# Optimization experiments

Measured on AMD Instinct MI355X. Metric: run time of the kernel, lower is better.

The kernel has to match this reference:

```python
import jax, jax.numpy as jnp
import numpy as np

# output_shape = (batch, channels, ny, nx)
B, C, NY, NX = 16, 64, 400, 400
NV_PER_BATCH = 12000  # non-empty pillars per frame (typical PointPillars)


def setup_inputs() -> dict:
    rng = np.random.default_rng(0)
    # unique pillar cells per batch -> deterministic scatter (matches torch last-write)
    cells = np.stack([rng.choice(NY * NX, NV_PER_BATCH, replace=False) for _ in range(B)])  # (B, NV)
    b_col = np.repeat(np.arange(B), NV_PER_BATCH)
    y = (cells // NX).reshape(-1)
    x = (cells % NX).reshape(-1)
    z = np.zeros_like(x)
    batched_indices = jnp.asarray(np.stack([b_col, z, y, x], axis=1), dtype=jnp.int32)  # (N, 4)
    voxel_features = jax.random.normal(jax.random.key(0), (B * NV_PER_BATCH, C), dtype=jnp.float32)
    return {"voxel_features": voxel_features, "batched_indices": batched_indices}


def reference(voxel_features, batched_indices):
    # fused global flat index: (batch, y, x) -> b*ny*nx + y*nx + x
    b = batched_indices[:, 0].astype(jnp.int32)
    y = batched_indices[:, 2].astype(jnp.int32)
    x = batched_indices[:, 3].astype(jnp.int32)
    flat = b * (NY * NX) + y * NX + x  # (N,)
    canvas = jnp.zeros((B * NY * NX, voxel_features.shape[1]), dtype=voxel_features.dtype)
    canvas = canvas.at[flat].set(voxel_features, unique_indices=True)
    # (B*NY*NX, C) -> (B, C, NY, NX)
    return canvas.reshape(B, NY, NX, -1).transpose(0, 3, 1, 2)
```

## Files before the change

kernel.cpp:

```cpp
#include <hip/hip_runtime.h>


constexpr int BATCH = 16;
constexpr int CH    = 64;
constexpr int NYD   = 400;
constexpr int NXD   = 400;
constexpr int NYNX  = NYD * NXD;
constexpr int SLABS = 8;
constexpr int CPS   = CH / SLABS;
constexpr int TILE  = 2048;

typedef float f4 __attribute__((ext_vector_type(4)));

__global__ void scatter_map_kernel(const int4* __restrict__ idx,
                                   unsigned short* __restrict__ map, int n, int nv) {
    int i = blockIdx.x * blockDim.x + threadIdx.x;
    if (i < n) {
        int4 v = idx[i];
        map[v.x * NYNX + v.z * NXD + v.w] = (unsigned short)(i - v.x * nv);
    }
}

__global__ __launch_bounds__(256)
void gather_kernel(const float* __restrict__ feat,
                   const unsigned short* __restrict__ map,
                   float* __restrict__ out, int nv) {
    const int b    = blockIdx.y;
    const int c0   = blockIdx.z * CPS;
    const int base = blockIdx.x * TILE + threadIdx.x * 4;

    const unsigned short* mapb  = map + (size_t)b * NYNX;
    const float*          featb = feat + ((size_t)b * nv) * CH + c0;
    float*                outb  = out + ((size_t)b * CH + c0) * NYNX;
    const f4 z4 = {0.f, 0.f, 0.f, 0.f};

    bool gv[2];
    unsigned short js[2][4];
    f4 f[2][4][2];
    #pragma unroll
    for (int g = 0; g < 2; ++g) {
        const int yx = base + g * 1024;
        gv[g] = (yx < NYNX);
        ushort4 m = gv[g] ? *reinterpret_cast<const ushort4*>(mapb + yx)
                          : make_ushort4(0xFFFFu, 0xFFFFu, 0xFFFFu, 0xFFFFu);
        js[g][0] = m.x; js[g][1] = m.y; js[g][2] = m.z; js[g][3] = m.w;
        #pragma unroll
        for (int cc = 0; cc < 4; ++cc) {
            if (js[g][cc] != 0xFFFFu) {
                const f4* src = reinterpret_cast<const f4*>(featb + (size_t)js[g][cc] * CH);
                f[g][cc][0] = src[0];
                f[g][cc][1] = src[1];
            } else {
                f[g][cc][0] = z4;
                f[g][cc][1] = z4;
            }
        }
    }

    #pragma unroll
    for (int g = 0; g < 2; ++g) {
        if (!gv[g]) continue;
        const int yx = base + g * 1024;
        #pragma unroll
        for (int k = 0; k < 2; ++k) {
            f4 r0 = {f[g][0][k].x, f[g][1][k].x, f[g][2][k].x, f[g][3][k].x};
            f4 r1 = {f[g][0][k].y, f[g][1][k].y, f[g][2][k].y, f[g][3][k].y};
            f4 r2 = {f[g][0][k].z, f[g][1][k].z, f[g][2][k].z, f[g][3][k].z};
            f4 r3 = {f[g][0][k].w, f[g][1][k].w, f[g][2][k].w, f[g][3][k].w};
            __builtin_nontemporal_store(r0, reinterpret_cast<f4*>(outb + (size_t)(4 * k + 0) * NYNX + yx));
            __builtin_nontemporal_store(r1, reinterpret_cast<f4*>(outb + (size_t)(4 * k + 1) * NYNX + yx));
            __builtin_nontemporal_store(r2, reinterpret_cast<f4*>(outb + (size_t)(4 * k + 2) * NYNX + yx));
            __builtin_nontemporal_store(r3, reinterpret_cast<f4*>(outb + (size_t)(4 * k + 3) * NYNX + yx));
        }
    }
}

__global__ void zero_kernel(float4* __restrict__ out, int n4) {
    int i = blockIdx.x * blockDim.x + threadIdx.x;
    if (i < n4) out[i] = make_float4(0.f, 0.f, 0.f, 0.f);
}

__global__ void direct_scatter_kernel(const float* __restrict__ feat,
                                      const int4* __restrict__ idx,
                                      float* __restrict__ out, int n) {
    int i = blockIdx.x * (blockDim.x / CH) + threadIdx.x / CH;
    int c = threadIdx.x % CH;
    if (i < n) {
        int4 v = idx[i];
        out[(size_t)(v.x * CH + c) * NYNX + v.z * NXD + v.w] = feat[(size_t)i * CH + c];
    }
}

extern "C" void kernel_launch(void* const* d_in, const int* in_sizes, int n_in,
                              void* d_out, int out_size, void* d_ws, size_t ws_size,
                              hipStream_t stream) {
    const float* feat = (const float*)d_in[0];
    const int4*  idx  = (const int4*)d_in[1];
    float*       out  = (float*)d_out;
    const int n  = in_sizes[1] / 4;
    const int nv = n / BATCH;

    const size_t map_bytes = (size_t)BATCH * NYNX * sizeof(unsigned short);
    if (ws_size >= map_bytes && nv < 0xFFFF) {
        unsigned short* map = (unsigned short*)d_ws;
        (void)hipMemsetAsync(map, 0xFF, map_bytes, stream);
        scatter_map_kernel<<<(n + 255) / 256, 256, 0, stream>>>(idx, map, n, nv);
        dim3 grid((NYNX + TILE - 1) / TILE, BATCH, SLABS);
        gather_kernel<<<grid, 256, 0, stream>>>(feat, map, out, nv);
    } else {
        int n4 = out_size / 4;
        zero_kernel<<<(n4 + 255) / 256, 256, 0, stream>>>((float4*)out, n4);
        direct_scatter_kernel<<<(n + 3) / 4, 256, 0, stream>>>(feat, idx, out, n);
    }
}
```

Measured before the change: 670.7 us.

## Loop over all channel slabs per thread with double-buffered feature loads

The gather kernel no longer splits channels across grid z. Each thread now reads its four map entries once and walks all eight channel slabs, prefetching the next slab's features into a second register buffer while storing the current slab. The tile shrinks to one group of 1024 cells per block. This removes the eight-fold redundant map reads and should keep gathered rows in cache across slabs, at the cost of fewer blocks, more registers per thread and a longer serial loop per thread.

```diff
diff --git a/kernel.cpp b/kernel.cpp
--- a/kernel.cpp
+++ b/kernel.cpp
@@ -8,7 +8,7 @@
 constexpr int NYNX  = NYD * NXD;
 constexpr int SLABS = 8;
 constexpr int CPS   = CH / SLABS;
-constexpr int TILE  = 2048;
+constexpr int TILE  = 1024;
 
 typedef float f4 __attribute__((ext_vector_type(4)));
 
@@ -25,52 +25,63 @@
 void gather_kernel(const float* __restrict__ feat,
                    const unsigned short* __restrict__ map,
                    float* __restrict__ out, int nv) {
-    const int b    = blockIdx.y;
-    const int c0   = blockIdx.z * CPS;
-    const int base = blockIdx.x * TILE + threadIdx.x * 4;
+    const int b  = blockIdx.y;
+    const int yx = blockIdx.x * TILE + threadIdx.x * 4;
+    if (yx >= NYNX) return;
 
-    const unsigned short* mapb  = map + (size_t)b * NYNX;
-    const float*          featb = feat + ((size_t)b * nv) * CH + c0;
-    float*                outb  = out + ((size_t)b * CH + c0) * NYNX;
+    const unsigned short* mapb  = map  + (size_t)b * NYNX;
+    const float*          featb = feat + ((size_t)b * nv) * CH;
+    float*                outb  = out  + (size_t)b * CH * NYNX + yx;
     const f4 z4 = {0.f, 0.f, 0.f, 0.f};
 
-    bool gv[2];
-    unsigned short js[2][4];
-    f4 f[2][4][2];
+    const ushort4 m = *reinterpret_cast<const ushort4*>(mapb + yx);
+    const unsigned short js[4] = {m.x, m.y, m.z, m.w};
+
+    f4 fA[4][2], fB[4][2];
+
     #pragma unroll
-    for (int g = 0; g < 2; ++g) {
-        const int yx = base + g * 1024;
-        gv[g] = (yx < NYNX);
-        ushort4 m = gv[g] ? *reinterpret_cast<const ushort4*>(mapb + yx)
-                          : make_ushort4(0xFFFFu, 0xFFFFu, 0xFFFFu, 0xFFFFu);
-        js[g][0] = m.x; js[g][1] = m.y; js[g][2] = m.z; js[g][3] = m.w;
-        #pragma unroll
-        for (int cc = 0; cc < 4; ++cc) {
-            if (js[g][cc] != 0xFFFFu) {
-                const f4* src = reinterpret_cast<const f4*>(featb + (size_t)js[g][cc] * CH);
-                f[g][cc][0] = src[0];
-                f[g][cc][1] = src[1];
-            } else {
-                f[g][cc][0] = z4;
-                f[g][cc][1] = z4;
-            }
+    for (int cc = 0; cc < 4; ++cc) {
+        if (js[cc] != 0xFFFFu) {
+            const f4* src = reinterpret_cast<const f4*>(featb + (size_t)js[cc] * CH);
+            fA[cc][0] = src[0];
+            fA[cc][1] = src[1];
+        } else {
+            fA[cc][0] = z4;
+            fA[cc][1] = z4;
         }
     }
 
     #pragma unroll
-    for (int g = 0; g < 2; ++g) {
-        if (!gv[g]) continue;
-        const int yx = base + g * 1024;
+    for (int s = 0; s < SLABS; ++s) {
+        f4 (*cur)[2] = (s & 1) ? fB : fA;
+        f4 (*nxt)[2] = (s & 1) ? fA : fB;
+
+        if (s + 1 < SLABS) {
+            #pragma unroll
+            for (int cc = 0; cc < 4; ++cc) {
+                if (js[cc] != 0xFFFFu) {
+                    const f4* src = reinterpret_cast<const f4*>(
+                        featb + (size_t)js[cc] * CH + (s + 1) * CPS);
+                    nxt[cc][0] = src[0];
+                    nxt[cc][1] = src[1];
+                } else {
+                    nxt[cc][0] = z4;
+                    nxt[cc][1] = z4;
+                }
+            }
+        }
+
+        float* outs = outb + (size_t)s * CPS * NYNX;
         #pragma unroll
         for (int k = 0; k < 2; ++k) {
-            f4 r0 = {f[g][0][k].x, f[g][1][k].x, f[g][2][k].x, f[g][3][k].x};
-            f4 r1 = {f[g][0][k].y, f[g][1][k].y, f[g][2][k].y, f[g][3][k].y};
-            f4 r2 = {f[g][0][k].z, f[g][1][k].z, f[g][2][k].z, f[g][3][k].z};
-            f4 r3 = {f[g][0][k].w, f[g][1][k].w, f[g][2][k].w, f[g][3][k].w};
-            __builtin_nontemporal_store(r0, reinterpret_cast<f4*>(outb + (size_t)(4 * k + 0) * NYNX + yx));
-            __builtin_nontemporal_store(r1, reinterpret_cast<f4*>(outb + (size_t)(4 * k + 1) * NYNX + yx));
-            __builtin_nontemporal_store(r2, reinterpret_cast<f4*>(outb + (size_t)(4 * k + 2) * NYNX + yx));
-            __builtin_nontemporal_store(r3, reinterpret_cast<f4*>(outb + (size_t)(4 * k + 3) * NYNX + yx));
+            f4 r0 = {cur[0][k].x, cur[1][k].x, cur[2][k].x, cur[3][k].x};
+            f4 r1 = {cur[0][k].y, cur[1][k].y, cur[2][k].y, cur[3][k].y};
+            f4 r2 = {cur[0][k].z, cur[1][k].z, cur[2][k].z, cur[3][k].z};
+            f4 r3 = {cur[0][k].w, cur[1][k].w, cur[2][k].w, cur[3][k].w};
+            __builtin_nontemporal_store(r0, reinterpret_cast<f4*>(outs + (size_t)(4 * k + 0) * NYNX));
+            __builtin_nontemporal_store(r1, reinterpret_cast<f4*>(outs + (size_t)(4 * k + 1) * NYNX));
+            __builtin_nontemporal_store(r2, reinterpret_cast<f4*>(outs + (size_t)(4 * k + 2) * NYNX));
+            __builtin_nontemporal_store(r3, reinterpret_cast<f4*>(outs + (size_t)(4 * k + 3) * NYNX));
         }
     }
 }
@@ -105,7 +116,7 @@
         unsigned short* map = (unsigned short*)d_ws;
         (void)hipMemsetAsync(map, 0xFF, map_bytes, stream);
         scatter_map_kernel<<<(n + 255) / 256, 256, 0, stream>>>(idx, map, n, nv);
-        dim3 grid((NYNX + TILE - 1) / TILE, BATCH, SLABS);
+        dim3 grid((NYNX + TILE - 1) / TILE, BATCH, 1);
         gather_kernel<<<grid, 256, 0, stream>>>(feat, map, out, nv);
     } else {
         int n4 = out_size / 4;
```

Measured after the change: 688.6 us. +2.7%, slower.
